# Kernel tuning notes

Hardware: AMD Instinct MI355X
Metric: run time of the kernel (lower is better)

The kernel has to match this reference:

```python
import jax, jax.numpy as jnp
import numpy as np

H = 16
D = 1024
DK = D // H


def setup_inputs() -> dict:
    key = jax.random.key(0)
    ks = jax.random.split(key, 10)
    B, S = 2, 2048
    scale = 1.0 / np.sqrt(D)
    inp = {
        "query": jax.random.normal(ks[0], (B, S, D), jnp.float32),
        "key_": jax.random.normal(ks[1], (B, S, D), jnp.float32),
        "value": jax.random.normal(ks[2], (B, S, D), jnp.float32),
        "Wq": jax.random.normal(ks[3], (D, D), jnp.float32) * scale,
        "bq": jnp.zeros((D,), jnp.float32),
        "Wk": jax.random.normal(ks[4], (D, D), jnp.float32) * scale,
        "bk": jnp.zeros((D,), jnp.float32),
        "Wv": jax.random.normal(ks[5], (D, D), jnp.float32) * scale,
        "bv": jnp.zeros((D,), jnp.float32),
        "ln_gamma": jnp.ones((D,), jnp.float32),
        "ln_beta": jnp.zeros((D,), jnp.float32),
    }
    return inp


def reference(query, key_, value, Wq, bq, Wk, bk, Wv, bv, ln_gamma, ln_beta):
    B, S, _ = query.shape
    residual = query
    # projections, split into heads: [B, H, S, DK]
    def proj(x, W, b):
        return (x @ W + b).reshape(B, -1, H, DK).transpose(0, 2, 1, 3)
    q = proj(query, Wq, bq)
    k = proj(key_, Wk, bk)
    v = proj(value, Wv, bv)
    # scaled dot-product attention with full score matrix (as in source)
    scores = jnp.einsum("bhqd,bhkd->bhqk", q, k) / jnp.sqrt(jnp.float32(DK))
    p_att = jax.nn.softmax(scores, axis=-1)  # dropout p=0 -> identity
    x = jnp.einsum("bhqk,bhkd->bhqd", p_att, v)
    x = x.transpose(0, 2, 1, 3).reshape(B, S, D)
    # residual + LayerNorm(eps=1e-6)
    y = x + residual
    mu = jnp.mean(y, axis=-1, keepdims=True)
    var = jnp.var(y, axis=-1, keepdims=True)
    y = (y - mu) / jnp.sqrt(var + 1e-6)
    return y * ln_gamma + ln_beta
```

## Files before the change

kernel.cpp:

```cpp
#include <hip/hip_runtime.h>


typedef float f32x4 __attribute__((ext_vector_type(4)));
typedef short short8 __attribute__((ext_vector_type(8)));
typedef unsigned int uint32x4 __attribute__((ext_vector_type(4)));

__device__ __forceinline__ unsigned short f2bf(float f) {
    unsigned u = __builtin_bit_cast(unsigned, f);
    u += 0x7fffu + ((u >> 16) & 1u);
    return (unsigned short)(u >> 16);
}
__device__ __forceinline__ unsigned packbf2(float lo, float hi) {
    return __builtin_amdgcn_perm(__builtin_bit_cast(unsigned, hi),
                                 __builtin_bit_cast(unsigned, lo), 0x07060302u);
}

__device__ __forceinline__ void g2l16(const unsigned short* g, unsigned short* l) {
    __builtin_amdgcn_global_load_lds(
        (const __attribute__((address_space(1))) unsigned int*)g,
        (__attribute__((address_space(3))) unsigned int*)l, 16, 0, 0);
}

__global__ __launch_bounds__(256) void convert_all(
    const float* __restrict__ xq, const float* __restrict__ xk, const float* __restrict__ xv,
    const float* __restrict__ Wq, const float* __restrict__ Wk, const float* __restrict__ Wv,
    unsigned short* __restrict__ xout, unsigned short* __restrict__ wout)
{
    const int bx  = blockIdx.x;
    const int tid = threadIdx.x;
    if (bx < 6144) {
        const int z = bx >> 11;
        const float* src = (z == 0) ? xq : (z == 1) ? xk : xv;
        const size_t idx = ((size_t)(bx & 2047) * 256 + tid) * 8;
        const float4 a = *(const float4*)(src + idx);
        const float4 b = *(const float4*)(src + idx + 4);
        short8 o;
        o[0] = (short)f2bf(a.x); o[1] = (short)f2bf(a.y);
        o[2] = (short)f2bf(a.z); o[3] = (short)f2bf(a.w);
        o[4] = (short)f2bf(b.x); o[5] = (short)f2bf(b.y);
        o[6] = (short)f2bf(b.z); o[7] = (short)f2bf(b.w);
        *(short8*)(xout + (size_t)z * 4194304 + idx) = o;
    } else {
        const int i = bx - 6144;
        const int z = i >> 8, tile = i & 255;
        const float* W = (z == 0) ? Wq : (z == 1) ? Wk : Wv;
        unsigned short* Wt = wout + (size_t)z * 1048576;
        __shared__ unsigned short Ts[64 * 65];
        const int kb0 = (tile >> 4) * 64, nb0 = (tile & 15) * 64;
        const int a = tid >> 6, b = tid & 63;
#pragma unroll
        for (int j = 0; j < 16; ++j) {
            const int k = j * 4 + a, n = b;
            Ts[n * 65 + k] = f2bf(W[(size_t)(kb0 + k) * 1024 + nb0 + n]);
        }
        __syncthreads();
#pragma unroll
        for (int j = 0; j < 16; ++j) {
            const int n = j * 4 + a, k = b;
            Wt[(size_t)(nb0 + n) * 1024 + kb0 + k] = Ts[n * 65 + k];
        }
    }
}

__global__ __launch_bounds__(256) void qkv_gemm(
    const unsigned short* __restrict__ Xb, const unsigned short* __restrict__ Wtb,
    const float* __restrict__ bq, const float* __restrict__ bk, const float* __restrict__ bv,
    unsigned short* __restrict__ qo, unsigned short* __restrict__ ko, unsigned short* __restrict__ vo)
{
    const int z = blockIdx.z;
    const unsigned short* X  = Xb  + (size_t)z * 4194304;
    const unsigned short* Wt = Wtb + (size_t)z * 1048576;
    const float* bias   = (z == 0) ? bq : (z == 1) ? bk : bv;
    unsigned short* out = (z == 0) ? qo : (z == 1) ? ko : vo;

    __shared__ unsigned short smem[16384];

    const int tid  = threadIdx.x;
    const int wave = tid >> 6;
    const int lane = tid & 63;
    const int l15  = lane & 15;
    const int quad = lane >> 4;
    const int mq   = wave & 1, nq = wave >> 1;
    const int mbase = blockIdx.x * 128, nbase = blockIdx.y * 128;

    const int srow = lane >> 2;
    const int schk = (lane & 3) ^ (srow & 3);

    const unsigned short* srcA = X  + (size_t)(mbase + wave * 32 + srow) * 1024 + schk * 8;
    const unsigned short* srcB = Wt + (size_t)(nbase + wave * 32 + srow) * 1024 + schk * 8;

    f32x4 acc[4][4];
#pragma unroll
    for (int i = 0; i < 4; ++i)
#pragma unroll
        for (int j = 0; j < 4; ++j) acc[i][j] = (f32x4){0.f, 0.f, 0.f, 0.f};

#pragma unroll
    for (int t = 0; t < 2; ++t) {
        g2l16(srcA + (size_t)t * 16 * 1024, &smem[(wave * 32 + t * 16) * 32]);
        g2l16(srcB + (size_t)t * 16 * 1024, &smem[4096 + (wave * 32 + t * 16) * 32]);
    }

    for (int it = 0; it < 32; ++it) {
        const int boff = (it & 1) * 8192;
        __syncthreads();

        if (it + 1 < 32) {
            const int poff = boff ^ 8192;
            const size_t ko2 = (size_t)(it + 1) * 32;
#pragma unroll
            for (int t = 0; t < 2; ++t) {
                g2l16(srcA + (size_t)t * 16 * 1024 + ko2, &smem[poff + (wave * 32 + t * 16) * 32]);
                g2l16(srcB + (size_t)t * 16 * 1024 + ko2, &smem[poff + 4096 + (wave * 32 + t * 16) * 32]);
            }
        }

        short8 af[4], bf[4];
#pragma unroll
        for (int i = 0; i < 4; ++i) {
            af[i] = *(const short8*)(&smem[boff + (mq * 64 + i * 16 + l15) * 32 + ((quad ^ (l15 & 3)) << 3)]);
            bf[i] = *(const short8*)(&smem[boff + 4096 + (nq * 64 + i * 16 + l15) * 32 + ((quad ^ (l15 & 3)) << 3)]);
        }
#pragma unroll
        for (int mt = 0; mt < 4; ++mt)
#pragma unroll
            for (int nt = 0; nt < 4; ++nt)
                acc[mt][nt] = __builtin_amdgcn_mfma_f32_16x16x32_bf16(af[mt], bf[nt], acc[mt][nt], 0, 0, 0);
    }

    __syncthreads();

    float bvals[4];
#pragma unroll
    for (int nt = 0; nt < 4; ++nt) bvals[nt] = bias[nbase + nq * 64 + nt * 16 + l15];

    if (z == 2) {
        unsigned short* Epv = smem;
        const int hbase = nbase >> 6;
        const int b     = mbase >> 11;
        const int srow0 = mbase & 2047;
#pragma unroll
        for (int nt = 0; nt < 4; ++nt) {
            __syncthreads();
            short8 w[2];
#pragma unroll
            for (int e = 0; e < 2; ++e)
#pragma unroll
                for (int j = 0; j < 8; ++j) {
                    const int mt2 = 2 * e + (j >> 2), r = j & 3;
                    w[e][j] = (short)f2bf(acc[mt2][nt][r] + bvals[nt]);
                }
            unsigned short* dst = &Epv[(nq * 16 + l15) * 136 + mq * 64 + quad * 8];
            *(short8*)(dst)      = w[0];
            *(short8*)(dst + 32) = w[1];
            __syncthreads();
            const int row = tid >> 3;
            const int d   = nt * 16 + (row & 15);
            const int h   = hbase + (row >> 4);
#pragma unroll
            for (int e = 0; e < 2; ++e) {
                const int colb = e * 64 + (tid & 7) * 8;
                short8 v = *(const short8*)(&Epv[row * 136 + colb]);
                *(short8*)(&out[((size_t)(b * 16 + h) * 64 + d) * 2048 + srow0 + colb]) = v;
            }
        }
    } else {
        unsigned short* Ep = smem + wave * 1152;
        const int hQ = (nbase + nq * 64) >> 6;
        const float scl = (z == 0) ? 0.18033688f : 1.0f;
#pragma unroll
        for (int mt = 0; mt < 4; ++mt) {
#pragma unroll
            for (int nt = 0; nt < 4; ++nt)
#pragma unroll
                for (int r = 0; r < 4; ++r)
                    Ep[(quad * 4 + r) * 72 + nt * 16 + l15] =
                        f2bf((acc[mt][nt][r] + bvals[nt]) * scl);
#pragma unroll
            for (int half = 0; half < 2; ++half) {
                const int m = (lane >> 3) + half * 8;
                const int nblk = lane & 7;
                short8 v = *(const short8*)(&Ep[m * 72 + nblk * 8]);
                const int gm = mbase + mq * 64 + mt * 16 + m;
                const int b2 = gm >> 11, srw = gm & 2047;
                *(short8*)(&out[((size_t)(b2 * 16 + hQ) * 2048 + srw) * 64 + nblk * 8]) = v;
            }
        }
    }
}

__global__ __launch_bounds__(512, 4) void attn(
    const unsigned short* __restrict__ qb, const unsigned short* __restrict__ kb,
    const unsigned short* __restrict__ vtb, float* __restrict__ xw)
{
    const int tid  = threadIdx.x;
    const int wave = tid >> 6;
    const int wq   = wave & 3;
    const int kvh  = wave >> 2;
    const int lane = tid & 63;
    const int l15  = lane & 15;
    const int quad = lane >> 4;

    const int bh    = blockIdx.x;
    const int qbase = blockIdx.y * 128 + wq * 32;

    __shared__ __align__(16) unsigned short smem[32768];
    __shared__ float Lsh[8][32];

    unsigned short* Ks0 = smem + kvh * 16384;
    unsigned short* Vs0 = Ks0 + 8192;

    short8 qf[2][2];
#pragma unroll
    for (int nt = 0; nt < 2; ++nt) {
        const unsigned short* Qp = qb + ((size_t)bh * 2048 + qbase + nt * 16 + l15) * 64 + quad * 8;
        qf[nt][0] = *(const short8*)(Qp);
        qf[nt][1] = *(const short8*)(Qp + 32);
    }

    const unsigned short* Kbh = kb  + ((size_t)bh * 2048 + (size_t)kvh * 1024) * 64;
    const unsigned short* Vbh = vtb + (size_t)bh * 64 * 2048 + (size_t)kvh * 1024;

    const int r8 = lane >> 3, c8 = lane & 7;
    const unsigned short *srcK[2], *srcV[2];
#pragma unroll
    for (int t = 0; t < 2; ++t) {
        const int row = wq * 16 + t * 8 + r8;
        srcK[t] = Kbh + (size_t)row * 64   + ((c8 ^ r8) << 3);
        srcV[t] = Vbh + (size_t)row * 2048 + ((c8 ^ r8) << 3);
    }

    uint32x4 ou; ou[0] = ou[1] = ou[2] = ou[3] = 0x3F803F80u;
    const short8 onesf = __builtin_bit_cast(short8, ou);

    f32x4 lacc[2];
    f32x4 O[2][4];
#pragma unroll
    for (int nt = 0; nt < 2; ++nt) {
        lacc[nt] = (f32x4){0.f, 0.f, 0.f, 0.f};
#pragma unroll
        for (int i = 0; i < 4; ++i) O[nt][i] = (f32x4){0.f, 0.f, 0.f, 0.f};
    }

#pragma unroll
    for (int t = 0; t < 2; ++t) {
        g2l16(srcK[t], Ks0 + (wq * 16 + t * 8) * 64);
        g2l16(srcV[t], Vs0 + (wq * 16 + t * 8) * 64);
    }

    for (int it = 0; it < 16; ++it) {
        const int buf = it & 1;
        __syncthreads();

        if (it + 1 < 16) {
            const size_t kn = (size_t)(it + 1) * 64;
#pragma unroll
            for (int t = 0; t < 2; ++t) {
                g2l16(srcK[t] + kn * 64, Ks0 + (buf ^ 1) * 4096 + (wq * 16 + t * 8) * 64);
                g2l16(srcV[t] + kn,      Vs0 + (buf ^ 1) * 4096 + (wq * 16 + t * 8) * 64);
            }
        }

        const unsigned short* Kb_ = Ks0 + buf * 4096;
        const unsigned short* Vb_ = Vs0 + buf * 4096;

        short8 kf[4][2];
#pragma unroll
        for (int mt = 0; mt < 4; ++mt)
#pragma unroll
            for (int dc = 0; dc < 2; ++dc)
                kf[mt][dc] = *(const short8*)(&Kb_[(mt * 16 + l15) * 64 +
                                                  ((((dc << 2) + quad) ^ (l15 & 7)) << 3)]);

        f32x4 sc[4][2];
#pragma unroll
        for (int mt = 0; mt < 4; ++mt)
#pragma unroll
            for (int nt = 0; nt < 2; ++nt) {
                f32x4 a = {0.f, 0.f, 0.f, 0.f};
                a = __builtin_amdgcn_mfma_f32_16x16x32_bf16(kf[mt][0], qf[nt][0], a, 0, 0, 0);
                a = __builtin_amdgcn_mfma_f32_16x16x32_bf16(kf[mt][1], qf[nt][1], a, 0, 0, 0);
                sc[mt][nt] = a;
            }

#pragma unroll
        for (int mt = 0; mt < 4; ++mt)
#pragma unroll
            for (int nt = 0; nt < 2; ++nt)
#pragma unroll
                for (int r = 0; r < 4; ++r)
                    sc[mt][nt][r] = __builtin_amdgcn_exp2f(sc[mt][nt][r]);

#pragma unroll
        for (int c = 0; c < 2; ++c) {
            short8 pf[2];
#pragma unroll
            for (int nt = 0; nt < 2; ++nt) {
                uint32x4 pu;
                pu[0] = packbf2(sc[2 * c][nt][0],     sc[2 * c][nt][1]);
                pu[1] = packbf2(sc[2 * c][nt][2],     sc[2 * c][nt][3]);
                pu[2] = packbf2(sc[2 * c + 1][nt][0], sc[2 * c + 1][nt][1]);
                pu[3] = packbf2(sc[2 * c + 1][nt][2], sc[2 * c + 1][nt][3]);
                pf[nt] = __builtin_bit_cast(short8, pu);
            }
            lacc[0] = __builtin_amdgcn_mfma_f32_16x16x32_bf16(onesf, pf[0], lacc[0], 0, 0, 0);
            lacc[1] = __builtin_amdgcn_mfma_f32_16x16x32_bf16(onesf, pf[1], lacc[1], 0, 0, 0);
#pragma unroll
            for (int dt = 0; dt < 4; ++dt) {
                const short8 vf = *(const short8*)(&Vb_[(dt * 16 + l15) * 64 +
                                                       ((((c << 2) + quad) ^ (l15 & 7)) << 3)]);
                O[0][dt] = __builtin_amdgcn_mfma_f32_16x16x32_bf16(vf, pf[0], O[0][dt], 0, 0, 0);
                O[1][dt] = __builtin_amdgcn_mfma_f32_16x16x32_bf16(vf, pf[1], O[1][dt], 0, 0, 0);
            }
        }
    }

    __syncthreads();

    if (quad == 0) {
        Lsh[wave][l15]      = lacc[0][0];
        Lsh[wave][16 + l15] = lacc[1][0];
    }

    float* Ow = (float*)smem + wave * 2048;
#pragma unroll
    for (int nt = 0; nt < 2; ++nt)
#pragma unroll
        for (int dt = 0; dt < 4; ++dt) {
            const int row  = nt * 16 + l15;
            const int c4s  = (dt * 4 + quad) ^ l15;
            *(f32x4*)(&Ow[row * 64 + c4s * 4]) = O[nt][dt];
        }
    __syncthreads();

    const float* OwA = (float*)smem + wq * 2048;
    const float* OwB = (float*)smem + (wq + 4) * 2048;
    const int b = bh >> 4, h = bh & 15;
    const size_t obase = ((size_t)b * 2048 + qbase) * 1024 + h * 64 + lane;
#pragma unroll
    for (int j = 0; j < 16; ++j) {
        const int qq   = kvh * 16 + j;
        const float li = 1.0f / (Lsh[wq][qq] + Lsh[wq + 4][qq]);
        const int off  = qq * 64 + (((lane >> 2) ^ (qq & 15)) << 2) + (lane & 3);
        xw[obase + (size_t)qq * 1024] = (OwA[off] + OwB[off]) * li;
    }
}

__global__ __launch_bounds__(256) void ln_kernel(
    const float* __restrict__ xw, const float* __restrict__ res,
    const float* __restrict__ gamma, const float* __restrict__ beta,
    float* __restrict__ out)
{
    const int row = blockIdx.x;
    const int tid = threadIdx.x;
    const size_t base = (size_t)row * 1024 + tid * 4;

    const float4 x  = *(const float4*)(xw + base);
    const float4 rv = *(const float4*)(res + base);
    float4 y;
    y.x = x.x + rv.x; y.y = x.y + rv.y; y.z = x.z + rv.z; y.w = x.w + rv.w;

    float s  = y.x + y.y + y.z + y.w;
    float s2 = y.x * y.x + y.y * y.y + y.z * y.z + y.w * y.w;
#pragma unroll
    for (int off = 32; off >= 1; off >>= 1) {
        s  += __shfl_xor(s, off);
        s2 += __shfl_xor(s2, off);
    }
    __shared__ float red[8];
    const int wave = tid >> 6;
    if ((tid & 63) == 0) { red[wave] = s; red[4 + wave] = s2; }
    __syncthreads();
    s  = red[0] + red[1] + red[2] + red[3];
    s2 = red[4] + red[5] + red[6] + red[7];

    const float mu   = s * (1.0f / 1024.0f);
    const float var  = s2 * (1.0f / 1024.0f) - mu * mu;
    const float rstd = rsqrtf(var + 1e-6f);

    const float4 g  = *(const float4*)(gamma + tid * 4);
    const float4 bt = *(const float4*)(beta + tid * 4);
    float4 o;
    o.x = (y.x - mu) * rstd * g.x + bt.x;
    o.y = (y.y - mu) * rstd * g.y + bt.y;
    o.z = (y.z - mu) * rstd * g.z + bt.z;
    o.w = (y.w - mu) * rstd * g.w + bt.w;
    *(float4*)(out + base) = o;
}

extern "C" void kernel_launch(void* const* d_in, const int* in_sizes, int n_in,
                              void* d_out, int out_size, void* d_ws, size_t ws_size,
                              hipStream_t stream) {
    const float* query = (const float*)d_in[0];
    const float* key_  = (const float*)d_in[1];
    const float* value = (const float*)d_in[2];
    const float* Wq    = (const float*)d_in[3];
    const float* bq    = (const float*)d_in[4];
    const float* Wk    = (const float*)d_in[5];
    const float* bk    = (const float*)d_in[6];
    const float* Wv    = (const float*)d_in[7];
    const float* bv    = (const float*)d_in[8];
    const float* ln_g  = (const float*)d_in[9];
    const float* ln_b  = (const float*)d_in[10];
    float* out = (float*)d_out;

    const size_t MB = 1024 * 1024;
    char* ws = (char*)d_ws;
    unsigned short* Xbuf = (unsigned short*)(ws);
    float*          xwp  = (float*)(ws);
    unsigned short* Wtb  = (unsigned short*)(ws + 24 * MB);
    unsigned short* qbuf = (unsigned short*)(ws + 30 * MB);
    unsigned short* kbuf = (unsigned short*)(ws + 38 * MB);
    unsigned short* vtb  = (unsigned short*)(ws + 46 * MB);

    convert_all<<<6912,           256, 0, stream>>>(query, key_, value, Wq, Wk, Wv, Xbuf, Wtb);
    qkv_gemm   <<<dim3(32, 8, 3), 256, 0, stream>>>(Xbuf, Wtb, bq, bk, bv, qbuf, kbuf, vtb);
    attn       <<<dim3(32, 16),   512, 0, stream>>>(qbuf, kbuf, vtb, xwp);
    ln_kernel  <<<4096,           256, 0, stream>>>(xwp, query, ln_g, ln_b, out);
}
```

Before: 201.8 us.

## Fuse activation fp32-to-bf16 conversion into QKV GEMM A-tile loading

The separate conversion pass over the query/key/value activations is removed. The GEMM now loads fp32 activations straight into registers, converts them to bf16, and stores them into the swizzled LDS tile after the MFMA loop, so the load latency overlaps with compute. This avoids writing and re-reading a 24MB bf16 activation buffer. In exchange, the GEMM reads fp32 A data again for each N-block (8x), uses more registers, and replaces the async global-to-LDS path with ordinary loads and stores.

Measured after the change: 196.3 us. 2.7% less time.

```diff
diff --git a/kernel.cpp b/kernel.cpp
--- a/kernel.cpp
+++ b/kernel.cpp
@@ -21,54 +21,48 @@
         (__attribute__((address_space(3))) unsigned int*)l, 16, 0, 0);
 }
 
-__global__ __launch_bounds__(256) void convert_all(
+__device__ __forceinline__ void cvt_store8(unsigned short* d, float4 a, float4 b) {
+    short8 o;
+    o[0] = (short)f2bf(a.x); o[1] = (short)f2bf(a.y);
+    o[2] = (short)f2bf(a.z); o[3] = (short)f2bf(a.w);
+    o[4] = (short)f2bf(b.x); o[5] = (short)f2bf(b.y);
+    o[6] = (short)f2bf(b.z); o[7] = (short)f2bf(b.w);
+    *(short8*)d = o;
+}
+
+__global__ __launch_bounds__(256) void convert_w(
+    const float* __restrict__ Wq, const float* __restrict__ Wk, const float* __restrict__ Wv,
+    unsigned short* __restrict__ wout)
+{
+    const int i = blockIdx.x;
+    const int tid = threadIdx.x;
+    const int z = i >> 8, tile = i & 255;
+    const float* W = (z == 0) ? Wq : (z == 1) ? Wk : Wv;
+    unsigned short* Wt = wout + (size_t)z * 1048576;
+    __shared__ unsigned short Ts[64 * 65];
+    const int kb0 = (tile >> 4) * 64, nb0 = (tile & 15) * 64;
+    const int a = tid >> 6, b = tid & 63;
+#pragma unroll
+    for (int j = 0; j < 16; ++j) {
+        const int k = j * 4 + a, n = b;
+        Ts[n * 65 + k] = f2bf(W[(size_t)(kb0 + k) * 1024 + nb0 + n]);
+    }
+    __syncthreads();
+#pragma unroll
+    for (int j = 0; j < 16; ++j) {
+        const int n = j * 4 + a, k = b;
+        Wt[(size_t)(nb0 + n) * 1024 + kb0 + k] = Ts[n * 65 + k];
+    }
+}
+
+__global__ __launch_bounds__(256) void qkv_gemm(
     const float* __restrict__ xq, const float* __restrict__ xk, const float* __restrict__ xv,
-    const float* __restrict__ Wq, const float* __restrict__ Wk, const float* __restrict__ Wv,
-    unsigned short* __restrict__ xout, unsigned short* __restrict__ wout)
-{
-    const int bx  = blockIdx.x;
-    const int tid = threadIdx.x;
-    if (bx < 6144) {
-        const int z = bx >> 11;
-        const float* src = (z == 0) ? xq : (z == 1) ? xk : xv;
-        const size_t idx = ((size_t)(bx & 2047) * 256 + tid) * 8;
-        const float4 a = *(const float4*)(src + idx);
-        const float4 b = *(const float4*)(src + idx + 4);
-        short8 o;
-        o[0] = (short)f2bf(a.x); o[1] = (short)f2bf(a.y);
-        o[2] = (short)f2bf(a.z); o[3] = (short)f2bf(a.w);
-        o[4] = (short)f2bf(b.x); o[5] = (short)f2bf(b.y);
-        o[6] = (short)f2bf(b.z); o[7] = (short)f2bf(b.w);
-        *(short8*)(xout + (size_t)z * 4194304 + idx) = o;
-    } else {
-        const int i = bx - 6144;
-        const int z = i >> 8, tile = i & 255;
-        const float* W = (z == 0) ? Wq : (z == 1) ? Wk : Wv;
-        unsigned short* Wt = wout + (size_t)z * 1048576;
-        __shared__ unsigned short Ts[64 * 65];
-        const int kb0 = (tile >> 4) * 64, nb0 = (tile & 15) * 64;
-        const int a = tid >> 6, b = tid & 63;
-#pragma unroll
-        for (int j = 0; j < 16; ++j) {
-            const int k = j * 4 + a, n = b;
-            Ts[n * 65 + k] = f2bf(W[(size_t)(kb0 + k) * 1024 + nb0 + n]);
-        }
-        __syncthreads();
-#pragma unroll
-        for (int j = 0; j < 16; ++j) {
-            const int n = j * 4 + a, k = b;
-            Wt[(size_t)(nb0 + n) * 1024 + kb0 + k] = Ts[n * 65 + k];
-        }
-    }
-}
-
-__global__ __launch_bounds__(256) void qkv_gemm(
-    const unsigned short* __restrict__ Xb, const unsigned short* __restrict__ Wtb,
+    const unsigned short* __restrict__ Wtb,
     const float* __restrict__ bq, const float* __restrict__ bk, const float* __restrict__ bv,
     unsigned short* __restrict__ qo, unsigned short* __restrict__ ko, unsigned short* __restrict__ vo)
 {
     const int z = blockIdx.z;
-    const unsigned short* X  = Xb  + (size_t)z * 4194304;
+    const float* Xf = (z == 0) ? xq : (z == 1) ? xk : xv;
     const unsigned short* Wt = Wtb + (size_t)z * 1048576;
     const float* bias   = (z == 0) ? bq : (z == 1) ? bk : bv;
     unsigned short* out = (z == 0) ? qo : (z == 1) ? ko : vo;
@@ -86,7 +80,11 @@
     const int srow = lane >> 2;
     const int schk = (lane & 3) ^ (srow & 3);
 
-    const unsigned short* srcA = X  + (size_t)(mbase + wave * 32 + srow) * 1024 + schk * 8;
+    const float* srcA0 = Xf + (size_t)(mbase + wave * 32 + srow) * 1024 + schk * 8;
+    const float* srcA1 = srcA0 + 16 * 1024;
+    unsigned short* dstA0 = &smem[(wave * 32 + srow) * 32 + (lane & 3) * 8];
+    unsigned short* dstA1 = dstA0 + 16 * 32;
+
     const unsigned short* srcB = Wt + (size_t)(nbase + wave * 32 + srow) * 1024 + schk * 8;
 
     f32x4 acc[4][4];
@@ -96,23 +94,32 @@
         for (int j = 0; j < 4; ++j) acc[i][j] = (f32x4){0.f, 0.f, 0.f, 0.f};
 
 #pragma unroll
-    for (int t = 0; t < 2; ++t) {
-        g2l16(srcA + (size_t)t * 16 * 1024, &smem[(wave * 32 + t * 16) * 32]);
+    for (int t = 0; t < 2; ++t)
         g2l16(srcB + (size_t)t * 16 * 1024, &smem[4096 + (wave * 32 + t * 16) * 32]);
+    {
+        const float4 x0 = *(const float4*)(srcA0);
+        const float4 x1 = *(const float4*)(srcA0 + 4);
+        const float4 y0 = *(const float4*)(srcA1);
+        const float4 y1 = *(const float4*)(srcA1 + 4);
+        cvt_store8(dstA0, x0, x1);
+        cvt_store8(dstA1, y0, y1);
     }
 
     for (int it = 0; it < 32; ++it) {
         const int boff = (it & 1) * 8192;
+        const int poff = boff ^ 8192;
         __syncthreads();
 
+        float4 a0, a1, c0, c1;
         if (it + 1 < 32) {
-            const int poff = boff ^ 8192;
             const size_t ko2 = (size_t)(it + 1) * 32;
 #pragma unroll
-            for (int t = 0; t < 2; ++t) {
-                g2l16(srcA + (size_t)t * 16 * 1024 + ko2, &smem[poff + (wave * 32 + t * 16) * 32]);
+            for (int t = 0; t < 2; ++t)
                 g2l16(srcB + (size_t)t * 16 * 1024 + ko2, &smem[poff + 4096 + (wave * 32 + t * 16) * 32]);
-            }
+            a0 = *(const float4*)(srcA0 + ko2);
+            a1 = *(const float4*)(srcA0 + ko2 + 4);
+            c0 = *(const float4*)(srcA1 + ko2);
+            c1 = *(const float4*)(srcA1 + ko2 + 4);
         }
 
         short8 af[4], bf[4];
@@ -126,6 +133,11 @@
 #pragma unroll
             for (int nt = 0; nt < 4; ++nt)
                 acc[mt][nt] = __builtin_amdgcn_mfma_f32_16x16x32_bf16(af[mt], bf[nt], acc[mt][nt], 0, 0, 0);
+
+        if (it + 1 < 32) {
+            cvt_store8(dstA0 + poff, a0, a1);
+            cvt_store8(dstA1 + poff, c0, c1);
+        }
     }
 
     __syncthreads();
@@ -406,15 +418,14 @@
 
     const size_t MB = 1024 * 1024;
     char* ws = (char*)d_ws;
-    unsigned short* Xbuf = (unsigned short*)(ws);
     float*          xwp  = (float*)(ws);
     unsigned short* Wtb  = (unsigned short*)(ws + 24 * MB);
     unsigned short* qbuf = (unsigned short*)(ws + 30 * MB);
     unsigned short* kbuf = (unsigned short*)(ws + 38 * MB);
     unsigned short* vtb  = (unsigned short*)(ws + 46 * MB);
 
-    convert_all<<<6912,           256, 0, stream>>>(query, key_, value, Wq, Wk, Wv, Xbuf, Wtb);
-    qkv_gemm   <<<dim3(32, 8, 3), 256, 0, stream>>>(Xbuf, Wtb, bq, bk, bv, qbuf, kbuf, vtb);
+    convert_w  <<<768,            256, 0, stream>>>(Wq, Wk, Wv, Wtb);
+    qkv_gemm   <<<dim3(32, 8, 3), 256, 0, stream>>>(query, key_, value, Wtb, bq, bk, bv, qbuf, kbuf, vtb);
     attn       <<<dim3(32, 16),   512, 0, stream>>>(qbuf, kbuf, vtb, xwp);
     ln_kernel  <<<4096,           256, 0, stream>>>(xwp, query, ln_g, ln_b, out);
 }
```
